# Optimization experiments

Measured on AMD Instinct MI355X. Metric: run time of the kernel, lower is better.

## Reference

```python
import jax, jax.numpy as jnp
import numpy as np

B, S, D, H, L, V = 2, 2048, 768, 12, 2, 32000
DH = D // H
DF = 4 * D
LN_EPS = 1e-5


def _pos_enc():
    # faithful to source: exponent uses 2*i/D with i already stepping by 2
    pos = jnp.arange(S, dtype=jnp.float32)[:, None]
    i = jnp.arange(0, D, 2, dtype=jnp.float32)
    ang = pos / (10000.0 ** (2.0 * i / D))
    enc = jnp.zeros((S, D), jnp.float32)
    enc = enc.at[:, 0::2].set(jnp.sin(ang)).at[:, 1::2].set(jnp.cos(ang))
    return enc


def _ln(x, g, b):
    m = jnp.mean(x, axis=-1, keepdims=True)
    v = jnp.mean((x - m) ** 2, axis=-1, keepdims=True)
    return (x - m) / jnp.sqrt(v + LN_EPS) * g + b


def _layer(x, p):
    Wq, bq, Wk, bk, Wv, bv, Wo, bo, g1, be1, W1, b1, W2, b2, g2, be2 = p
    q = (x @ Wq + bq).reshape(B, S, H, DH)
    k = (x @ Wk + bk).reshape(B, S, H, DH)
    v = (x @ Wv + bv).reshape(B, S, H, DH)
    # NOTE: source divides by sqrt(embed_dim), not sqrt(head_dim)
    attn = jnp.einsum('bqhd,bkhd->bhqk', q, k) / jnp.sqrt(jnp.float32(D))
    attn = jax.nn.softmax(attn, axis=-1)  # [B,H,S,S]
    o = jnp.einsum('bhqk,bkhd->bqhd', attn, v).reshape(B, S, D)
    o = o @ Wo + bo
    x = _ln(x + o, g1, be1)
    h = jax.nn.gelu(x @ W1 + b1, approximate=False)
    x = _ln(x + h @ W2 + b2, g2, be2)
    return x


def setup_inputs() -> dict:
    key = jax.random.key(0)
    ks = jax.random.split(key, 16)
    n = lambda k, shape: jax.random.normal(k, shape, dtype=jnp.float32) * 0.02
    return {
        'input_ids': jax.random.randint(ks[0], (B, S), 0, V),
        'embed_table': n(ks[1], (V, D)),
        'Wq': n(ks[2], (L, D, D)), 'bq': jnp.zeros((L, D), jnp.float32),
        'Wk': n(ks[3], (L, D, D)), 'bk': jnp.zeros((L, D), jnp.float32),
        'Wv': n(ks[4], (L, D, D)), 'bv': jnp.zeros((L, D), jnp.float32),
        'Wo': n(ks[5], (L, D, D)), 'bo': jnp.zeros((L, D), jnp.float32),
        'ln1_g': jnp.ones((L, D), jnp.float32), 'ln1_b': jnp.zeros((L, D), jnp.float32),
        'W1': n(ks[6], (L, D, DF)), 'b1': jnp.zeros((L, DF), jnp.float32),
        'W2': n(ks[7], (L, DF, D)), 'b2': jnp.zeros((L, D), jnp.float32),
        'ln2_g': jnp.ones((L, D), jnp.float32), 'ln2_b': jnp.zeros((L, D), jnp.float32),
        'Wd': n(ks[8], (D, D)), 'bd': jnp.zeros((D,), jnp.float32),
        'lnm_g': jnp.ones((D,), jnp.float32), 'lnm_b': jnp.zeros((D,), jnp.float32),
        'dec_b': jnp.zeros((V,), jnp.float32),
    }


def reference(input_ids, embed_table, Wq, bq, Wk, bk, Wv, bv, Wo, bo,
              ln1_g, ln1_b, W1, b1, W2, b2, ln2_g, ln2_b,
              Wd, bd, lnm_g, lnm_b, dec_b):
    x = embed_table[input_ids] + _pos_enc()[None]  # [B,S,D]

    def step(h, p):
        return _layer(h, p), None

    x, _ = jax.lax.scan(step, x, (Wq, bq, Wk, bk, Wv, bv, Wo, bo,
                                  ln1_g, ln1_b, W1, b1, W2, b2, ln2_g, ln2_b))
    # MLM head with decoder weight tied to embedding table
    h = jax.nn.gelu(x @ Wd + bd, approximate=False)
    h = _ln(h, lnm_g, lnm_b)
    return h @ embed_table.T + dec_b  # [B,S,V]
```

## Files before the change

### kernel.cpp

```cpp
#include <hip/hip_runtime.h>
#include <hip/hip_bf16.h>
#include <cstdint>

typedef __bf16 bf16x8 __attribute__((ext_vector_type(8)));
typedef float  f32x4  __attribute__((ext_vector_type(4)));
typedef unsigned short u16;
typedef u16 u16x8 __attribute__((ext_vector_type(8)));

__device__ __forceinline__ u16 f2bf(float f) {
    union { float f; uint32_t u; } x{f};
    uint32_t u = x.u;
    return (u16)((u + 0x7fffu + ((u >> 16) & 1u)) >> 16);
}

__device__ __forceinline__ float fexp2(float x) {
    return __builtin_amdgcn_exp2f(x);
}

__device__ __forceinline__ float gelu_f(float x) {
    return 0.5f * x * (1.0f + erff(x * 0.70710678118654752f));
}

__device__ __forceinline__ void gl_lds16(const void* g, void* l) {
    __builtin_amdgcn_global_load_lds(
        (__attribute__((address_space(1))) void*)(void*)g,
        (__attribute__((address_space(3))) void*)l, 16, 0, 0);
}

#define MFMA16(a, b, c) __builtin_amdgcn_mfma_f32_16x16x32_bf16((a), (b), (c), 0, 0, 0)
#define SB0 __builtin_amdgcn_sched_barrier(0)

template<int EPI, int OUTF32, int LOC, int SPLITK, int QS>
__global__ __launch_bounds__(256, 2) void gemm_bf16(
    const u16* __restrict__ A, const u16* __restrict__ Bt,
    const float* __restrict__ bias, void* __restrict__ Cout,
    int N_, int K_, float qs)
{
    __shared__ u16 lA[128 * 64];
    __shared__ u16 lB[128 * 64];
    const int tid  = threadIdx.x;
    const int lane = tid & 63;
    const int wave = tid >> 6;
    const int wr = wave >> 1, wc = wave & 1;
    long row0, col0;
    if (LOC) {
        const int bid = blockIdx.x;
        const int chunk = bid >> 9, rem = bid & 511;
        row0 = (long)(rem & 31) * 128;
        col0 = (long)(chunk * 16 + (rem >> 5)) * 128;
    } else {
        row0 = (long)blockIdx.y * 128;
        col0 = (long)blockIdx.x * 128;
    }
    const int KS = K_ / SPLITK;
    const int kz = (SPLITK > 1) ? blockIdx.z * KS : 0;

    f32x4 acc[4][4];
#pragma unroll
    for (int i = 0; i < 4; ++i)
#pragma unroll
        for (int j = 0; j < 4; ++j)
#pragma unroll
            for (int t = 0; t < 4; ++t) acc[i][j][t] = 0.f;

    int sRow[4], sKb[4];
#pragma unroll
    for (int t = 0; t < 4; ++t) {
        int byteoff = (wave * 4 + t) * 1024 + lane * 16;
        int r = byteoff >> 7;
        sRow[t] = r;
        sKb[t]  = (byteoff & 127) ^ ((r & 7) << 4);
    }
    const int laneRC = lane & 15;
    const int laneK2 = (lane >> 4) * 16;

    for (int k0 = kz; k0 < kz + KS; k0 += 64) {
#pragma unroll
        for (int t = 0; t < 4; ++t) {
            const int cb = (wave * 4 + t) * 1024;
            gl_lds16(A  + (row0 + sRow[t]) * K_ + k0 + (sKb[t] >> 1), (char*)lA + cb);
            gl_lds16(Bt + (col0 + sRow[t]) * K_ + k0 + (sKb[t] >> 1), (char*)lB + cb);
        }
        __syncthreads();
#pragma unroll
        for (int kk = 0; kk < 2; ++kk) {
            bf16x8 af[4], bfr[4];
#pragma unroll
            for (int i = 0; i < 4; ++i) {
                int r = wr * 64 + i * 16 + laneRC;
                af[i] = *(const bf16x8*)((const char*)lA + r * 128 + ((kk * 64 + laneK2) ^ ((r & 7) << 4)));
            }
#pragma unroll
            for (int j = 0; j < 4; ++j) {
                int n = wc * 64 + j * 16 + laneRC;
                bfr[j] = *(const bf16x8*)((const char*)lB + n * 128 + ((kk * 64 + laneK2) ^ ((n & 7) << 4)));
            }
#pragma unroll
            for (int i = 0; i < 4; ++i)
#pragma unroll
                for (int j = 0; j < 4; ++j)
                    acc[i][j] = MFMA16(af[i], bfr[j], acc[i][j]);
        }
        __syncthreads();
    }

    float* outF = (float*)Cout + (SPLITK > 1 ? (long)blockIdx.z * 4096 * N_ : 0);
    const float qmul = (QS && col0 < 768) ? qs : 1.0f;
#pragma unroll
    for (int j = 0; j < 4; ++j) {
        const long cidx = col0 + wc * 64 + j * 16 + laneRC;
        const float bvv = (SPLITK == 1 || blockIdx.z == 0) ? bias[cidx] : 0.f;
#pragma unroll
        for (int i = 0; i < 4; ++i) {
            const long rbase = row0 + wr * 64 + i * 16 + ((lane >> 4) << 2);
#pragma unroll
            for (int t = 0; t < 4; ++t) {
                float v = acc[i][j][t] + bvv;
                if (QS) v *= qmul;
                if (EPI) v = gelu_f(v);
                const long off = (rbase + t) * N_ + cidx;
                if (OUTF32) outF[off] = v;
                else        ((u16*)Cout)[off] = f2bf(v);
            }
        }
    }
}

template<int EPI, int OUTF32>
__global__ __launch_bounds__(256, 4) void gemm64(
    const u16* __restrict__ A, const u16* __restrict__ Bt,
    const float* __restrict__ bias, void* __restrict__ Cout,
    int N_, int K_)
{
    __shared__ u16 lA[64 * 64];
    __shared__ u16 lB[64 * 64];
    const int tid  = threadIdx.x;
    const int lane = tid & 63;
    const int wave = tid >> 6;
    const int wr = wave >> 1, wc = wave & 1;
    const long row0 = (long)blockIdx.y * 64;
    const long col0 = (long)blockIdx.x * 64;

    f32x4 acc[2][2];
#pragma unroll
    for (int i = 0; i < 2; ++i)
#pragma unroll
        for (int j = 0; j < 2; ++j)
#pragma unroll
            for (int t = 0; t < 4; ++t) acc[i][j][t] = 0.f;

    int sRow[2], sKb[2];
#pragma unroll
    for (int t = 0; t < 2; ++t) {
        int byteoff = (wave * 2 + t) * 1024 + lane * 16;
        int r = byteoff >> 7;
        sRow[t] = r;
        sKb[t]  = (byteoff & 127) ^ ((r & 7) << 4);
    }
    const int laneRC = lane & 15;
    const int laneK2 = (lane >> 4) * 16;

    for (int k0 = 0; k0 < K_; k0 += 64) {
#pragma unroll
        for (int t = 0; t < 2; ++t) {
            const int cb = (wave * 2 + t) * 1024;
            gl_lds16(A  + (row0 + sRow[t]) * K_ + k0 + (sKb[t] >> 1), (char*)lA + cb);
            gl_lds16(Bt + (col0 + sRow[t]) * K_ + k0 + (sKb[t] >> 1), (char*)lB + cb);
        }
        __syncthreads();
#pragma unroll
        for (int kk = 0; kk < 2; ++kk) {
            bf16x8 af[2], bfr[2];
#pragma unroll
            for (int i = 0; i < 2; ++i) {
                int r = wr * 32 + i * 16 + laneRC;
                af[i] = *(const bf16x8*)((const char*)lA + r * 128 + ((kk * 64 + laneK2) ^ ((r & 7) << 4)));
            }
#pragma unroll
            for (int j = 0; j < 2; ++j) {
                int n = wc * 32 + j * 16 + laneRC;
                bfr[j] = *(const bf16x8*)((const char*)lB + n * 128 + ((kk * 64 + laneK2) ^ ((n & 7) << 4)));
            }
#pragma unroll
            for (int i = 0; i < 2; ++i)
#pragma unroll
                for (int j = 0; j < 2; ++j)
                    acc[i][j] = MFMA16(af[i], bfr[j], acc[i][j]);
        }
        __syncthreads();
    }

#pragma unroll
    for (int j = 0; j < 2; ++j) {
        const long cidx = col0 + wc * 32 + j * 16 + laneRC;
        const float bvv = bias[cidx];
#pragma unroll
        for (int i = 0; i < 2; ++i) {
            const long rbase = row0 + wr * 32 + i * 16 + ((lane >> 4) << 2);
#pragma unroll
            for (int t = 0; t < 4; ++t) {
                float v = acc[i][j][t] + bvv;
                if (EPI) v = gelu_f(v);
                const long off = (rbase + t) * N_ + cidx;
                if (OUTF32) ((float*)Cout)[off] = v;
                else        ((u16*)Cout)[off]  = f2bf(v);
            }
        }
    }
}

__global__ __launch_bounds__(256, 4) void attn_fwd(
    const u16* __restrict__ qkv, u16* __restrict__ outb)
{
    __shared__ u16 lQP[64 * 64];
    __shared__ u16 lK[2][64 * 64];
    __shared__ u16 lVt[2][64 * 64];
    const int bh = blockIdx.x;
    const int b = bh / 12, h = bh % 12;
    const int q0 = blockIdx.y * 64;
    const int tid = threadIdx.x, lane = tid & 63, wave = tid >> 6;
    const long baseQ = (long)b * 2048 * 2304 + h * 64;
    const long baseK = baseQ + 768;
    const long baseV = baseQ + 1536;
    const int laneRC = lane & 15;
    const int laneK2 = (lane >> 4) * 16;

    int stR[2], stC[2];
#pragma unroll
    for (int t = 0; t < 2; ++t) {
        const int byteoff = (wave * 2 + t) * 1024 + lane * 16;
        const int r = byteoff >> 7;
        stR[t] = r;
        stC[t] = ((byteoff & 127) ^ ((r & 7) << 4)) >> 1;
    }

#define STAGEK(BUF, KB0) do {                                                    \
    _Pragma("unroll") for (int t = 0; t < 2; ++t)                                \
        gl_lds16(qkv + baseK + (long)((KB0) + stR[t]) * 2304 + stC[t],           \
                 (char*)lK[BUF] + (wave * 2 + t) * 1024);                        \
} while (0)

#pragma unroll
    for (int t = 0; t < 2; ++t)
        gl_lds16(qkv + baseQ + (long)(q0 + stR[t]) * 2304 + stC[t],
                 (char*)lQP + (wave * 2 + t) * 1024);
    STAGEK(0, 0);
    u16x8 vA0, vA1;
    {
        const u16x8* gv = (const u16x8*)(qkv + baseV + (long)lane * 2304 + wave * 16);
        vA0 = gv[0]; vA1 = gv[1];
    }
    __syncthreads();

    bf16x8 qf[2];
#pragma unroll
    for (int kk = 0; kk < 2; ++kk) {
        int r = wave * 16 + laneRC;
        qf[kk] = *(const bf16x8*)((const char*)lQP + r * 128 + ((kk * 64 + laneK2) ^ ((r & 7) << 4)));
    }

    bf16x8 onesf;
#pragma unroll
    for (int j = 0; j < 8; ++j) onesf[j] = (__bf16)1.0f;

    float mrun = -1e30f;
    f32x4 oacc[4], oaccS;
#pragma unroll
    for (int dc = 0; dc < 4; ++dc)
#pragma unroll
        for (int t = 0; t < 4; ++t) oacc[dc][t] = 0.f;
#pragma unroll
    for (int t = 0; t < 4; ++t) oaccS[t] = 0.f;

    u16x8 vB0 = vA0, vB1 = vA1;
    for (int kt = 0; kt < 32; ++kt) {
        const int cur = kt & 1;
        asm volatile("s_waitcnt vmcnt(0)" ::: "memory");
        SB0;
        {
            const int kv = lane, dg = wave;
            char* vt = (char*)lVt[cur];
#pragma unroll
            for (int j = 0; j < 8; ++j) {
                int d0 = dg * 16 + j;
                *(u16*)(vt + d0 * 128 + ((kv * 2) ^ ((d0 & 7) << 4))) = vA0[j];
                int d1 = dg * 16 + 8 + j;
                *(u16*)(vt + d1 * 128 + ((kv * 2) ^ ((d1 & 7) << 4))) = vA1[j];
            }
        }
        __builtin_amdgcn_s_barrier();
        SB0;
        if (kt + 1 < 32) {
            STAGEK(cur ^ 1, (kt + 1) * 64);
            const u16x8* gv = (const u16x8*)(qkv + baseV + (long)((kt + 1) * 64 + lane) * 2304 + wave * 16);
            vB0 = gv[0]; vB1 = gv[1];
        }
        const char* lKc = (const char*)lK[cur];
        const char* lVc = (const char*)lVt[cur];

        f32x4 s[4];
#pragma unroll
        for (int cb = 0; cb < 4; ++cb)
#pragma unroll
            for (int t = 0; t < 4; ++t) s[cb][t] = 0.f;
        __builtin_amdgcn_s_setprio(1);
#pragma unroll
        for (int kk = 0; kk < 2; ++kk) {
            bf16x8 kf[4];
#pragma unroll
            for (int cb = 0; cb < 4; ++cb) {
                int kr = cb * 16 + laneRC;
                kf[cb] = *(const bf16x8*)(lKc + kr * 128 + ((kk * 64 + laneK2) ^ ((kr & 7) << 4)));
            }
#pragma unroll
            for (int cb = 0; cb < 4; ++cb)
                s[cb] = MFMA16(kf[cb], qf[kk], s[cb]);
        }
        __builtin_amdgcn_s_setprio(0);

        if ((kt & 7) == 0) {
            float pmax = s[0][0];
#pragma unroll
            for (int cb = 0; cb < 4; ++cb)
#pragma unroll
                for (int r = 0; r < 4; ++r) pmax = fmaxf(pmax, s[cb][r]);
            pmax = fmaxf(pmax, __shfl_xor(pmax, 16, 64));
            pmax = fmaxf(pmax, __shfl_xor(pmax, 32, 64));
            if (__ballot(pmax - mrun > 8.0f)) {
                const float mnew = fmaxf(mrun, pmax);
                const float corr = fexp2(mrun - mnew);
                mrun = mnew;
#pragma unroll
                for (int dc = 0; dc < 4; ++dc)
#pragma unroll
                    for (int t = 0; t < 4; ++t) oacc[dc][t] *= corr;
#pragma unroll
                for (int t = 0; t < 4; ++t) oaccS[t] *= corr;
            }
        }

        {
            char* pbase = (char*)lQP + (wave * 16 + laneRC) * 128;
            const int pswz = (laneRC & 7) << 4;
            const int g8 = (lane >> 4) * 8;
#pragma unroll
            for (int c = 0; c < 4; ++c) {
                const uint32_t w0 = (uint32_t)f2bf(fexp2(s[c][0] - mrun))
                                  | ((uint32_t)f2bf(fexp2(s[c][1] - mrun)) << 16);
                const uint32_t w1 = (uint32_t)f2bf(fexp2(s[c][2] - mrun))
                                  | ((uint32_t)f2bf(fexp2(s[c][3] - mrun)) << 16);
                uint2 pk; pk.x = w0; pk.y = w1;
                *(uint2*)(pbase + ((c * 32 + g8) ^ pswz)) = pk;
            }
        }

        __builtin_amdgcn_s_setprio(1);
#pragma unroll
        for (int kk = 0; kk < 2; ++kk) {
            bf16x8 pf, vf[4];
            {
                int pr = wave * 16 + laneRC;
                pf = *(const bf16x8*)((const char*)lQP + pr * 128 + ((kk * 64 + laneK2) ^ ((pr & 7) << 4)));
            }
#pragma unroll
            for (int dc = 0; dc < 4; ++dc) {
                int d = dc * 16 + laneRC;
                vf[dc] = *(const bf16x8*)(lVc + d * 128 + ((kk * 64 + laneK2) ^ ((d & 7) << 4)));
            }
#pragma unroll
            for (int dc = 0; dc < 4; ++dc)
                oacc[dc] = MFMA16(vf[dc], pf, oacc[dc]);
            oaccS = MFMA16(onesf, pf, oaccS);
        }
        __builtin_amdgcn_s_setprio(0);
        vA0 = vB0; vA1 = vB1;
    }
#undef STAGEK

    const float inv = 1.0f / oaccS[0];
    const long rowq = (long)b * 2048 + q0 + wave * 16 + (lane & 15);
#pragma unroll
    for (int dc = 0; dc < 4; ++dc) {
        const int colb = h * 64 + dc * 16 + ((lane >> 4) << 2);
        ushort4 st;
        st.x = f2bf(oacc[dc][0] * inv);
        st.y = f2bf(oacc[dc][1] * inv);
        st.z = f2bf(oacc[dc][2] * inv);
        st.w = f2bf(oacc[dc][3] * inv);
        *(ushort4*)(outb + rowq * 768 + colb) = st;
    }
}

template<int NP>
__global__ __launch_bounds__(256) void ln_fused(
    const float* __restrict__ a, const float* __restrict__ parts, long pstride,
    const float* __restrict__ g, const float* __restrict__ be,
    float* __restrict__ outf, u16* __restrict__ outb)
{
    const int wave = threadIdx.x >> 6, lane = threadIdx.x & 63;
    const int row = blockIdx.x * 4 + wave;
    const size_t rbase = (size_t)row * 768;
    float4 v[3];
    float s1 = 0.f, s2 = 0.f;
#pragma unroll
    for (int i = 0; i < 3; ++i) {
        const int c = lane * 4 + i * 256;
        float4 x = *(const float4*)(a + rbase + c);
#pragma unroll
        for (int p = 0; p < NP; ++p) {
            const float4 y = *(const float4*)(parts + (size_t)p * pstride + rbase + c);
            x.x += y.x; x.y += y.y; x.z += y.z; x.w += y.w;
        }
        v[i] = x;
        s1 += x.x + x.y + x.z + x.w;
        s2 += x.x * x.x + x.y * x.y + x.z * x.z + x.w * x.w;
    }
#pragma unroll
    for (int m = 1; m < 64; m <<= 1) { s1 += __shfl_xor(s1, m, 64); s2 += __shfl_xor(s2, m, 64); }
    const float mean = s1 * (1.f / 768.f);
    const float var  = s2 * (1.f / 768.f) - mean * mean;
    const float rstd = rsqrtf(var + 1e-5f);
#pragma unroll
    for (int i = 0; i < 3; ++i) {
        const int c = lane * 4 + i * 256;
        const float4 gg = *(const float4*)(g + c);
        const float4 bb = *(const float4*)(be + c);
        float4 y;
        y.x = (v[i].x - mean) * rstd * gg.x + bb.x;
        y.y = (v[i].y - mean) * rstd * gg.y + bb.y;
        y.z = (v[i].z - mean) * rstd * gg.z + bb.z;
        y.w = (v[i].w - mean) * rstd * gg.w + bb.w;
        if (outf) *(float4*)(outf + rbase + c) = y;
        ushort4 u; u.x = f2bf(y.x); u.y = f2bf(y.y); u.z = f2bf(y.z); u.w = f2bf(y.w);
        *(ushort4*)(outb + rbase + c) = u;
    }
}

struct PrepArgs {
    const float* tsrc[13]; u16* tdst[13];
    const float* emb; u16* embB;
    const int* ids; float* xf; u16* xb;
    const float* bq; const float* bk; const float* bv; float* bqkv;
};
__global__ __launch_bounds__(256) void prep_all(PrepArgs pa)
{
    const int bid = blockIdx.x;
    if (bid < 14400) {
        int z, bx, by, R, C;
        if (bid < 5184)       { z = bid / 576;              int r = bid - z * 576;    bx = r % 24; by = r / 24; R = 768;  C = 768;  }
        else if (bid < 9792)  { z = 9 + (bid - 5184) / 2304;  int r = (bid - 5184) % 2304; bx = r % 96; by = r / 96; R = 768;  C = 3072; }
        else                  { z = 11 + (bid - 9792) / 2304; int r = (bid - 9792) % 2304; bx = r % 24; by = r / 24; R = 3072; C = 768;  }
        __shared__ float t[32][33];
        const float* in = pa.tsrc[z];
        u16* out = pa.tdst[z];
        const int c0 = bx * 32, r0 = by * 32;
        const int tx = threadIdx.x & 31, ty = threadIdx.x >> 5;
#pragma unroll
        for (int i = 0; i < 4; ++i)
            t[ty + 8 * i][tx] = in[(size_t)(r0 + ty + 8 * i) * C + c0 + tx];
        __syncthreads();
#pragma unroll
        for (int i = 0; i < 4; ++i)
            out[(size_t)(c0 + ty + 8 * i) * R + r0 + tx] = f2bf(t[tx][ty + 8 * i]);
        return;
    }
    const long A = 6144000;
    const long B = 3145728;
    long t = (long)(bid - 14400) * 256 + threadIdx.x;
    if (t < A) {
        const long i = t * 4;
        const float4 f = *(const float4*)(pa.emb + i);
        ushort4 u; u.x = f2bf(f.x); u.y = f2bf(f.y); u.z = f2bf(f.z); u.w = f2bf(f.w);
        *(ushort4*)(pa.embB + i) = u;
    } else if (t < A + B) {
        const int idx = (int)(t - A);
        const int row = idx / 768, d = idx - row * 768;
        const int s = row & 2047;
        const float e = pa.emb[(long)pa.ids[row] * 768 + d];
        const int j = d >> 1;
        const float ang = (float)s * __expf(-0.011992630692677324f * (float)(4 * j));
        const float pe = (d & 1) ? __cosf(ang) : __sinf(ang);
        const float v = e + pe;
        pa.xf[idx] = v;
        pa.xb[idx] = f2bf(v);
    } else {
        const int i = (int)(t - A - B);
        if (i < 4608) {
            int l = i / 2304, j = i - l * 2304;
            float v = (j < 768) ? pa.bq[l * 768 + j]
                    : (j < 1536) ? pa.bk[l * 768 + j - 768]
                    : pa.bv[l * 768 + j - 1536];
            pa.bqkv[i] = v;
        }
    }
}

extern "C" void kernel_launch(void* const* d_in, const int* in_sizes, int n_in,
                              void* d_out, int out_size, void* d_ws, size_t ws_size,
                              hipStream_t stream)
{
    const int S = 2048, D = 768, H = 12, L = 2, V = 32000, DF = 3072, M = 4096, NQKV = 2304;
    (void)in_sizes; (void)n_in; (void)out_size; (void)ws_size; (void)H; (void)S;

    const int*   ids  = (const int*)  d_in[0];
    const float* emb  = (const float*)d_in[1];
    const float* Wq   = (const float*)d_in[2];
    const float* bq   = (const float*)d_in[3];
    const float* Wk   = (const float*)d_in[4];
    const float* bk   = (const float*)d_in[5];
    const float* Wv   = (const float*)d_in[6];
    const float* bv   = (const float*)d_in[7];
    const float* Wo   = (const float*)d_in[8];
    const float* bo   = (const float*)d_in[9];
    const float* ln1g = (const float*)d_in[10];
    const float* ln1b = (const float*)d_in[11];
    const float* W1   = (const float*)d_in[12];
    const float* b1   = (const float*)d_in[13];
    const float* W2   = (const float*)d_in[14];
    const float* b2   = (const float*)d_in[15];
    const float* ln2g = (const float*)d_in[16];
    const float* ln2b = (const float*)d_in[17];
    const float* Wd   = (const float*)d_in[18];
    const float* bd   = (const float*)d_in[19];
    const float* lnmg = (const float*)d_in[20];
    const float* lnmb = (const float*)d_in[21];
    const float* decb = (const float*)d_in[22];

    char* p = (char*)d_ws;
    auto carve = [&](size_t bytes) { char* r = p; p += (bytes + 255) & ~(size_t)255; return r; };
    u16*   embB  = (u16*)  carve((size_t)V * D * 2);
    u16*   wqkvT = (u16*)  carve((size_t)L * NQKV * D * 2);
    float* bqkv  = (float*)carve((size_t)L * NQKV * 4);
    u16*   woT   = (u16*)  carve((size_t)L * D * D * 2);
    u16*   w1T   = (u16*)  carve((size_t)L * DF * D * 2);
    u16*   w2T   = (u16*)  carve((size_t)L * D * DF * 2);
    u16*   wdT   = (u16*)  carve((size_t)D * D * 2);
    float* xf    = (float*)carve((size_t)M * D * 4);
    u16*   xb    = (u16*)  carve((size_t)M * D * 2);
    u16*   qkvB  = (u16*)  carve((size_t)M * NQKV * 2);
    u16*   aoB   = (u16*)  carve((size_t)M * D * 2);
    float* tmpf  = (float*)carve((size_t)M * D * 4 * 4);
    u16*   hB    = (u16*)  carve((size_t)M * DF * 2);

    {
        PrepArgs pa;
        for (int l = 0; l < L; ++l) {
            pa.tsrc[l * 4 + 0] = Wq + (size_t)l * D * D; pa.tdst[l * 4 + 0] = wqkvT + (size_t)l * NQKV * D;
            pa.tsrc[l * 4 + 1] = Wk + (size_t)l * D * D; pa.tdst[l * 4 + 1] = wqkvT + (size_t)l * NQKV * D + (size_t)D * D;
            pa.tsrc[l * 4 + 2] = Wv + (size_t)l * D * D; pa.tdst[l * 4 + 2] = wqkvT + (size_t)l * NQKV * D + (size_t)2 * D * D;
            pa.tsrc[l * 4 + 3] = Wo + (size_t)l * D * D; pa.tdst[l * 4 + 3] = woT + (size_t)l * D * D;
        }
        pa.tsrc[8]  = Wd;                    pa.tdst[8]  = wdT;
        pa.tsrc[9]  = W1;                    pa.tdst[9]  = w1T;
        pa.tsrc[10] = W1 + (size_t)D * DF;   pa.tdst[10] = w1T + (size_t)DF * D;
        pa.tsrc[11] = W2;                    pa.tdst[11] = w2T;
        pa.tsrc[12] = W2 + (size_t)DF * D;   pa.tdst[12] = w2T + (size_t)D * DF;
        pa.emb = emb; pa.embB = embB;
        pa.ids = ids; pa.xf = xf; pa.xb = xb;
        pa.bq = bq; pa.bk = bk; pa.bv = bv; pa.bqkv = bqkv;
        prep_all<<<14400 + 36306, 256, 0, stream>>>(pa);
    }

    const float qscale = 0.036084391824351615f * 1.4426950408889634f;
    const long PSTR = (long)M * D;
    for (int l = 0; l < L; ++l) {
        gemm_bf16<0, 0, 0, 1, 1><<<dim3(NQKV / 128, M / 128), 256, 0, stream>>>(xb, wqkvT + (size_t)l * NQKV * D, bqkv + l * NQKV, qkvB, NQKV, D, qscale);
        attn_fwd<<<dim3(24, 32), 256, 0, stream>>>(qkvB, aoB);
        gemm64<0, 1><<<dim3(D / 64, M / 64), 256, 0, stream>>>(aoB, woT + (size_t)l * D * D, bo + l * D, tmpf, D, D);
        ln_fused<1><<<M / 4, 256, 0, stream>>>(xf, tmpf, PSTR, ln1g + l * D, ln1b + l * D, xf, xb);
        gemm_bf16<1, 0, 0, 1, 0><<<dim3(DF / 128, M / 128), 256, 0, stream>>>(xb, w1T + (size_t)l * DF * D, b1 + l * DF, hB, DF, D, 1.0f);
        gemm_bf16<0, 1, 0, 2, 0><<<dim3(D / 128, M / 128, 2), 256, 0, stream>>>(hB, w2T + (size_t)l * D * DF, b2 + l * D, tmpf, D, DF, 1.0f);
        ln_fused<2><<<M / 4, 256, 0, stream>>>(xf, tmpf, PSTR, ln2g + l * D, ln2b + l * D, xf, xb);
    }
    gemm64<1, 1><<<dim3(D / 64, M / 64), 256, 0, stream>>>(xb, wdT, bd, tmpf, D, D);
    ln_fused<0><<<M / 4, 256, 0, stream>>>(tmpf, nullptr, 0, lnmg, lnmb, nullptr, aoB);
    gemm_bf16<0, 1, 1, 1, 0><<<V / 128 * 32, 256, 0, stream>>>(aoB, embB, decb, (float*)d_out, V, D, 1.0f);
}
```

Baseline: 716.6 us.

## Use 128-row query tiles with 8 waves per attention block sharing K/V

The attention kernel now processes 128 query rows per block with 512 threads (8 waves) instead of 64 rows with 4 waves. Each staged K tile and transposed V tile in LDS is therefore reused by twice as many queries, halving K/V global traffic and per-block staging work. Each thread now loads one 16-byte K chunk and one V vector per tile instead of two. The grid shrinks to 384 blocks, which reduces parallelism on the device, and the larger Q buffer raises LDS use per block.

```diff
diff --git a/kernel.cpp b/kernel.cpp
--- a/kernel.cpp
+++ b/kernel.cpp
@@ -209,15 +209,15 @@
     }
 }
 
-__global__ __launch_bounds__(256, 4) void attn_fwd(
+__global__ __launch_bounds__(512, 4) void attn_fwd(
     const u16* __restrict__ qkv, u16* __restrict__ outb)
 {
-    __shared__ u16 lQP[64 * 64];
+    __shared__ u16 lQP[128 * 64];
     __shared__ u16 lK[2][64 * 64];
     __shared__ u16 lVt[2][64 * 64];
-    const int bh = blockIdx.x;
+    const int bh = blockIdx.y;
     const int b = bh / 12, h = bh % 12;
-    const int q0 = blockIdx.y * 64;
+    const int q0 = blockIdx.x * 128;
     const int tid = threadIdx.x, lane = tid & 63, wave = tid >> 6;
     const long baseQ = (long)b * 2048 * 2304 + h * 64;
     const long baseK = baseQ + 768;
@@ -225,31 +225,19 @@
     const int laneRC = lane & 15;
     const int laneK2 = (lane >> 4) * 16;
 
-    int stR[2], stC[2];
-#pragma unroll
-    for (int t = 0; t < 2; ++t) {
-        const int byteoff = (wave * 2 + t) * 1024 + lane * 16;
-        const int r = byteoff >> 7;
-        stR[t] = r;
-        stC[t] = ((byteoff & 127) ^ ((r & 7) << 4)) >> 1;
-    }
-
-#define STAGEK(BUF, KB0) do {                                                    \
-    _Pragma("unroll") for (int t = 0; t < 2; ++t)                                \
-        gl_lds16(qkv + baseK + (long)((KB0) + stR[t]) * 2304 + stC[t],           \
-                 (char*)lK[BUF] + (wave * 2 + t) * 1024);                        \
-} while (0)
-
-#pragma unroll
-    for (int t = 0; t < 2; ++t)
-        gl_lds16(qkv + baseQ + (long)(q0 + stR[t]) * 2304 + stC[t],
-                 (char*)lQP + (wave * 2 + t) * 1024);
+    const int kR = tid >> 3;
+    const int kC = (((tid & 7) * 16) ^ ((kR & 7) << 4)) >> 1;
+
+#define STAGEK(BUF, KB0) \
+    gl_lds16(qkv + baseK + (long)((KB0) + kR) * 2304 + kC, (char*)lK[BUF] + wave * 1024)
+
+#pragma unroll
+    for (int is = 0; is < 2; ++is)
+        gl_lds16(qkv + baseQ + (long)(q0 + is * 64 + kR) * 2304 + kC,
+                 (char*)lQP + is * 8192 + wave * 1024);
     STAGEK(0, 0);
-    u16x8 vA0, vA1;
-    {
-        const u16x8* gv = (const u16x8*)(qkv + baseV + (long)lane * 2304 + wave * 16);
-        vA0 = gv[0]; vA1 = gv[1];
-    }
+    u16x8 vA;
+    vA = *(const u16x8*)(qkv + baseV + (long)lane * 2304 + wave * 8);
     __syncthreads();
 
     bf16x8 qf[2];
@@ -272,28 +260,24 @@
 #pragma unroll
     for (int t = 0; t < 4; ++t) oaccS[t] = 0.f;
 
-    u16x8 vB0 = vA0, vB1 = vA1;
+    u16x8 vB = vA;
     for (int kt = 0; kt < 32; ++kt) {
         const int cur = kt & 1;
         asm volatile("s_waitcnt vmcnt(0)" ::: "memory");
         SB0;
         {
-            const int kv = lane, dg = wave;
             char* vt = (char*)lVt[cur];
 #pragma unroll
             for (int j = 0; j < 8; ++j) {
-                int d0 = dg * 16 + j;
-                *(u16*)(vt + d0 * 128 + ((kv * 2) ^ ((d0 & 7) << 4))) = vA0[j];
-                int d1 = dg * 16 + 8 + j;
-                *(u16*)(vt + d1 * 128 + ((kv * 2) ^ ((d1 & 7) << 4))) = vA1[j];
+                int d = wave * 8 + j;
+                *(u16*)(vt + d * 128 + ((lane * 2) ^ ((d & 7) << 4))) = vA[j];
             }
         }
         __builtin_amdgcn_s_barrier();
         SB0;
         if (kt + 1 < 32) {
             STAGEK(cur ^ 1, (kt + 1) * 64);
-            const u16x8* gv = (const u16x8*)(qkv + baseV + (long)((kt + 1) * 64 + lane) * 2304 + wave * 16);
-            vB0 = gv[0]; vB1 = gv[1];
+            vB = *(const u16x8*)(qkv + baseV + (long)((kt + 1) * 64 + lane) * 2304 + wave * 8);
         }
         const char* lKc = (const char*)lK[cur];
         const char* lVc = (const char*)lVt[cur];
@@ -373,7 +357,7 @@
             oaccS = MFMA16(onesf, pf, oaccS);
         }
         __builtin_amdgcn_s_setprio(0);
-        vA0 = vB0; vA1 = vB1;
+        vA = vB;
     }
 #undef STAGEK
 
@@ -565,7 +549,7 @@
     const long PSTR = (long)M * D;
     for (int l = 0; l < L; ++l) {
         gemm_bf16<0, 0, 0, 1, 1><<<dim3(NQKV / 128, M / 128), 256, 0, stream>>>(xb, wqkvT + (size_t)l * NQKV * D, bqkv + l * NQKV, qkvB, NQKV, D, qscale);
-        attn_fwd<<<dim3(24, 32), 256, 0, stream>>>(qkvB, aoB);
+        attn_fwd<<<dim3(16, 24), 512, 0, stream>>>(qkvB, aoB);
         gemm64<0, 1><<<dim3(D / 64, M / 64), 256, 0, stream>>>(aoB, woT + (size_t)l * D * D, bo + l * D, tmpf, D, D);
         ln_fused<1><<<M / 4, 256, 0, stream>>>(xf, tmpf, PSTR, ln1g + l * D, ln1b + l * D, xf, xb);
         gemm_bf16<1, 0, 0, 1, 0><<<dim3(DF / 128, M / 128), 256, 0, stream>>>(xb, w1T + (size_t)l * DF * D, b1 + l * DF, hB, DF, D, 1.0f);
```

New measurement: 722.0 us. About the same (+0.8%).
